# Kernel tuning notes

Measured on AMD Instinct MI355X. Metric: run time of the kernel, lower is better.

Reference implementation:

```python
import jax, jax.numpy as jnp
import numpy as np

N_NODES = 50000
N_EDGES = 1600000
IN_F, H_F, N_C = 128, 128, 16
NEG_SLOPE = 0.2  # DGL GATConv default


def setup_inputs() -> dict:
    key = jax.random.key(0)
    ks = jax.random.split(key, 12)
    def w(k, shape, fan_in):
        return jax.random.normal(k, shape, jnp.float32) / np.float32(np.sqrt(fan_in))
    return {
        "feat": jax.random.normal(ks[0], (N_NODES, IN_F), jnp.float32),
        "src": jax.random.randint(ks[1], (N_EDGES,), 0, N_NODES, dtype=jnp.int32),
        "dst": jax.random.randint(ks[2], (N_EDGES,), 0, N_NODES, dtype=jnp.int32),
        "W1": w(ks[3], (IN_F, H_F), IN_F), "al1": w(ks[4], (H_F,), H_F), "ar1": w(ks[5], (H_F,), H_F), "b1": jnp.zeros((H_F,), jnp.float32),
        "W2": w(ks[6], (H_F, H_F), H_F), "al2": w(ks[7], (H_F,), H_F), "ar2": w(ks[8], (H_F,), H_F), "b2": jnp.zeros((H_F,), jnp.float32),
        "W3": w(ks[9], (H_F, N_C), H_F), "al3": w(ks[10], (N_C,), N_C), "ar3": w(ks[11], (N_C,), N_C), "b3": jnp.zeros((N_C,), jnp.float32),
    }


def _gat_layer(h, src, dst, W, al, ar, b):
    # DGL GATConv (1 head): ft = W h; e_ij = LeakyReLU(a_l.ft_src + a_r.ft_dst);
    # alpha = edge_softmax over incoming edges of dst; out = sum alpha * ft_src + bias
    ft = h @ W                                   # [N, out]
    el = ft @ al                                 # [N]
    er = ft @ ar                                 # [N]
    e = jax.nn.leaky_relu(el[src] + er[dst], negative_slope=NEG_SLOPE)  # [E]
    emax = jax.ops.segment_max(e, dst, num_segments=N_NODES)
    emax = jnp.where(jnp.isfinite(emax), emax, 0.0)  # guard isolated nodes
    ex = jnp.exp(e - emax[dst])                  # [E]
    esum = jax.ops.segment_sum(ex, dst, num_segments=N_NODES)  # [N]
    agg = jax.ops.segment_sum(ex[:, None] * ft[src], dst, num_segments=N_NODES)  # [N, out]
    out = agg / jnp.where(esum > 0, esum, 1.0)[:, None] + b
    return jax.nn.relu(out)


def reference(feat, src, dst, W1, al1, ar1, b1, W2, al2, ar2, b2, W3, al3, ar3, b3):
    h = _gat_layer(feat, src, dst, W1, al1, ar1, b1)
    h = _gat_layer(h, src, dst, W2, al2, ar2, b2)
    h = _gat_layer(h, src, dst, W3, al3, ar3, b3)
    return h  # [N_NODES, N_C]
```

## Files before the change

### kernel.cpp

```cpp
#include <hip/hip_runtime.h>
#include <hip/hip_bf16.h>

#define NN 50000
#define NE 1600000
#define FF 128
#define CC 16
#define NB ((NN + 63) / 64)
#define NBLK 256
#define CH ((NE + NBLK - 1) / NBLK)

using bf16 = __hip_bfloat16;
using bf16x8 = __attribute__((ext_vector_type(8))) short;
using f32x4  = __attribute__((ext_vector_type(4))) float;

static __device__ __forceinline__ float ldf(const void* p, int i, int isbf){
    return isbf ? __bfloat162float(((const bf16*)p)[i]) : ((const float*)p)[i];
}
static __device__ __forceinline__ float bflo(unsigned u){
    union{unsigned x; float f;} c; c.x = u << 16; return c.f;
}
static __device__ __forceinline__ float bfhi(unsigned u){
    union{unsigned x; float f;} c; c.x = u & 0xFFFF0000u; return c.f;
}
static __device__ __forceinline__ unsigned short f2bfu(float v){
    bf16 b = __float2bfloat16(v);
    union{bf16 b; unsigned short u;} c; c.b = b; return c.u;
}

__global__ __launch_bounds__(256) void k_prep(const unsigned short* __restrict__ featu,
                                              const void* __restrict__ W1, const void* __restrict__ W2,
                                              const void* __restrict__ W3, int* __restrict__ dflag,
                                              int* __restrict__ bcounts, unsigned short* __restrict__ wtg){
    __shared__ int cnt;
    const int t = threadIdx.x;
    if (t == 0) cnt = 0;
    __syncthreads();
    unsigned short lo = featu[2 * t];
    int e = (lo >> 7) & 0xFF;
    if (e >= 117 && e <= 137) atomicAdd(&cnt, 1);
    __syncthreads();
    const int isbf = (cnt >= 128) ? 1 : 0;
    int idx = blockIdx.x * 256 + t;
    if (idx == 0) *dflag = isbf;
    if (idx < NB) bcounts[idx] = 0;
    if (idx < 32768){
        int l = idx >> 14;
        int e2 = idx & 16383;
        int f = e2 >> 7, k = e2 & 127;
        const void* W = l ? W2 : W1;
        wtg[idx] = f2bfu(ldf(W, k * FF + f, isbf));
    } else if (idx < 34816){
        int e2 = idx - 32768;
        int f = e2 >> 7, k = e2 & 127;
        wtg[idx] = f2bfu(ldf(W3, k * CC + f, isbf));
    }
}


__global__ __launch_bounds__(256) void k_bcount(const int* __restrict__ dst, int* __restrict__ bcounts,
                                                int* __restrict__ bh){
    __shared__ int hist[NB];
    const int t = threadIdx.x, b = blockIdx.x;
    for (int i = t; i < NB; i += 256) hist[i] = 0;
    __syncthreads();
    const int beg = b * CH, end = (beg + CH < NE) ? beg + CH : NE;
    for (int i = beg + t; i < end; i += 256){
        int d = dst[i];
        if ((unsigned)d >= NN) d = 0;
        atomicAdd(&hist[d >> 6], 1);
    }
    __syncthreads();
    for (int k = t; k < NB; k += 256){
        int v = hist[k];
        bh[k * NBLK + b] = v;
        if (v) atomicAdd(&bcounts[k], v);
    }
}

__global__ __launch_bounds__(256) void k_bscan(const int* __restrict__ bcounts, int* __restrict__ bbase,
                                               int* __restrict__ rowptr){
    __shared__ int s[256];
    const int t = threadIdx.x;
    constexpr int PT = (NB + 255) / 256;
    int loc[PT];
    int sum = 0;
    #pragma unroll
    for (int i = 0; i < PT; i++){
        int idx = t * PT + i;
        int v = (idx < NB) ? bcounts[idx] : 0;
        loc[i] = sum;
        sum += v;
    }
    s[t] = sum; __syncthreads();
    for (int off = 1; off < 256; off <<= 1){
        int x = (t >= off) ? s[t - off] : 0;
        __syncthreads();
        s[t] += x;
        __syncthreads();
    }
    int base = (t > 0) ? s[t - 1] : 0;
    #pragma unroll
    for (int i = 0; i < PT; i++){
        int idx = t * PT + i;
        if (idx < NB) bbase[idx] = base + loc[i];
    }
    if (t == 255){
        bbase[NB] = s[255];
        rowptr[NN] = s[255];
    }
}

__global__ __launch_bounds__(256) void k_boffset(const int* __restrict__ bbase, int* __restrict__ bh){
    int k = blockIdx.x * 4 + (threadIdx.x >> 6);
    int lane = threadIdx.x & 63;
    if (k >= NB) return;
    int v[4];
    int s = 0;
    #pragma unroll
    for (int i = 0; i < 4; i++){
        v[i] = bh[k * NBLK + 4 * lane + i];
        s += v[i];
    }
    int tot = s;
    #pragma unroll
    for (int off = 1; off < 64; off <<= 1){
        int x = __shfl_up(s, off);
        if (lane >= off) s += x;
    }
    int run = bbase[k] + s - tot;
    #pragma unroll
    for (int i = 0; i < 4; i++){
        bh[k * NBLK + 4 * lane + i] = run;
        run += v[i];
    }
}

__global__ __launch_bounds__(256) void k_bucket(const int* __restrict__ src, const int* __restrict__ dst,
                                                const int* __restrict__ bh, unsigned* __restrict__ bpairs){
    __shared__ int cur[NB];
    const int t = threadIdx.x, b = blockIdx.x;
    for (int k = t; k < NB; k += 256) cur[k] = bh[k * NBLK + b];
    __syncthreads();
    const int beg = b * CH, end = (beg + CH < NE) ? beg + CH : NE;
    for (int i = beg + t; i < end; i += 256){
        int s = src[i];
        int d = dst[i];
        if ((unsigned)s >= NN) s = 0;
        if ((unsigned)d >= NN) d = 0;
        int p = atomicAdd(&cur[d >> 6], 1);
        if ((unsigned)p < NE) bpairs[p] = (unsigned)s | ((unsigned)(d & 63) << 16);
    }
}

__global__ __launch_bounds__(256) void k_bsort(const unsigned* __restrict__ bpairs, const int* __restrict__ bbase,
                                               int* __restrict__ rowptr, int* __restrict__ csrsrc){
    __shared__ int cnt[64];
    __shared__ int cur[64];
    const int t = threadIdx.x;
    const int b = blockIdx.x;
    const int base = bbase[b];
    const int endb = bbase[b + 1];
    if (t < 64) cnt[t] = 0;
    __syncthreads();
    for (int i = base + t; i < endb; i += 256)
        atomicAdd(&cnt[bpairs[i] >> 16], 1);
    __syncthreads();
    if (t < 64){
        int v = cnt[t];
        int inc = v;
        #pragma unroll
        for (int off = 1; off < 64; off <<= 1){
            int x = __shfl_up(inc, off);
            if (t >= off) inc += x;
        }
        int excl = inc - v;
        cur[t] = excl;
        int d = b * 64 + t;
        if (d < NN) rowptr[d] = base + excl;
    }
    __syncthreads();
    for (int i = base + t; i < endb; i += 256){
        unsigned pr = bpairs[i];
        int p = atomicAdd(&cur[pr >> 16], 1);
        csrsrc[base + p] = (int)(pr & 0xFFFFu);
    }
}


template<bool XDYN>
__global__ __launch_bounds__(256) void k_mgemm(const void* __restrict__ X, const unsigned short* __restrict__ wtg,
                                               const void* __restrict__ al, const void* __restrict__ ar,
                                               const int* __restrict__ dflag, bf16* __restrict__ ft,
                                               float* __restrict__ el, float* __restrict__ er){
    const int isbf = *dflag;
    const int t  = threadIdx.x;
    const int n0 = blockIdx.x * 64;
    const int wv = t >> 6;
    const int lane = t & 63;
    const int quad = lane >> 4;
    const int mcol = lane & 15;
    const int row = n0 + wv * 16 + mcol;
    const int rc  = (row < NN) ? row : 0;

    bf16x8 afr[4];
    if (XDYN && !isbf){
        const float* xr = (const float*)X + rc * FF + quad * 8;
        #pragma unroll
        for (int kt = 0; kt < 4; kt++){
            float4 a = *(const float4*)(xr + kt * 32);
            float4 b = *(const float4*)(xr + kt * 32 + 4);
            union { bf16x8 v; unsigned u[4]; } c;
            c.u[0] = (unsigned)f2bfu(a.x) | ((unsigned)f2bfu(a.y) << 16);
            c.u[1] = (unsigned)f2bfu(a.z) | ((unsigned)f2bfu(a.w) << 16);
            c.u[2] = (unsigned)f2bfu(b.x) | ((unsigned)f2bfu(b.y) << 16);
            c.u[3] = (unsigned)f2bfu(b.z) | ((unsigned)f2bfu(b.w) << 16);
            afr[kt] = c.v;
        }
    } else {
        const unsigned short* xr = (const unsigned short*)X + rc * FF + quad * 8;
        #pragma unroll
        for (int kt = 0; kt < 4; kt++)
            afr[kt] = *(const bf16x8*)(xr + kt * 32);
    }

    float elp[4] = {0.f,0.f,0.f,0.f}, erp[4] = {0.f,0.f,0.f,0.f};

    #pragma unroll
    for (int f = 0; f < 8; f++){
        f32x4 acc = {0.f, 0.f, 0.f, 0.f};
        const unsigned short* wr = wtg + (f * 16 + mcol) * FF + quad * 8;
        #pragma unroll
        for (int kt = 0; kt < 4; kt++){
            bf16x8 bfr = *(const bf16x8*)(wr + kt * 32);
            acc = __builtin_amdgcn_mfma_f32_16x16x32_bf16(afr[kt], bfr, acc, 0, 0, 0);
        }
        int col = f * 16 + mcol;
        float alv = ldf(al, col, isbf);
        float arv = ldf(ar, col, isbf);
        #pragma unroll
        for (int reg = 0; reg < 4; reg++){
            int node = n0 + wv * 16 + quad * 4 + reg;
            float v = acc[reg];
            if (node < NN) ft[node * FF + col] = __float2bfloat16(v);
            elp[reg] += v * alv;
            erp[reg] += v * arv;
        }
    }

    #pragma unroll
    for (int reg = 0; reg < 4; reg++){
        float pl = elp[reg], pr = erp[reg];
        #pragma unroll
        for (int off = 1; off < 16; off <<= 1){
            pl += __shfl_xor(pl, off);
            pr += __shfl_xor(pr, off);
        }
        int node = n0 + wv * 16 + quad * 4 + reg;
        if (mcol == 0 && node < NN){ el[node] = pl; er[node] = pr; }
    }
}


__global__ __launch_bounds__(256) void k_mgemm3(const void* __restrict__ X, const unsigned short* __restrict__ wt3g,
                                                const void* __restrict__ al, const void* __restrict__ ar,
                                                const int* __restrict__ dflag, float* __restrict__ ft,
                                                float* __restrict__ el, float* __restrict__ er){
    const int isbf = *dflag;
    const int t  = threadIdx.x;
    const int n0 = blockIdx.x * 64;
    const int wv = t >> 6;
    const int lane = t & 63;
    const int quad = lane >> 4;
    const int mcol = lane & 15;
    const int row = n0 + wv * 16 + mcol;
    const int rc  = (row < NN) ? row : 0;

    const unsigned short* xr = (const unsigned short*)X + rc * FF + quad * 8;
    const unsigned short* wr = wt3g + mcol * FF + quad * 8;

    f32x4 acc = {0.f, 0.f, 0.f, 0.f};
    #pragma unroll
    for (int kt = 0; kt < 4; kt++){
        bf16x8 afr = *(const bf16x8*)(xr + kt * 32);
        bf16x8 bfr = *(const bf16x8*)(wr + kt * 32);
        acc = __builtin_amdgcn_mfma_f32_16x16x32_bf16(afr, bfr, acc, 0, 0, 0);
    }

    float alv = ldf(al, mcol, isbf);
    float arv = ldf(ar, mcol, isbf);
    #pragma unroll
    for (int reg = 0; reg < 4; reg++){
        int node = n0 + wv * 16 + quad * 4 + reg;
        float v = acc[reg];
        if (node < NN) ft[node * CC + mcol] = v;
        float pl = v * alv, pr = v * arv;
        #pragma unroll
        for (int off = 1; off < 16; off <<= 1){
            pl += __shfl_xor(pl, off);
            pr += __shfl_xor(pr, off);
        }
        if (mcol == 0 && node < NN){ el[node] = pl; er[node] = pr; }
    }
}


__global__ __launch_bounds__(256) void k_wnorm(const float* __restrict__ el, float* __restrict__ er,
                                               const int* __restrict__ rowptr, const int* __restrict__ csrsrc,
                                               float* __restrict__ wcsr){
    const int t = threadIdx.x;
    const int n = blockIdx.x * 64 + (t >> 2);
    if (n >= NN) return;
    const int sub = t & 3;
    int beg = rowptr[n], end = rowptr[n + 1];
    beg = (beg < 0) ? 0 : (beg > NE ? NE : beg);
    end = (end < beg) ? beg : (end > NE ? NE : end);
    const float erd = er[n];
    float sum = 0.f;
    for (int i = beg + sub; i < end; i += 4){
        int s = csrsrc[i];
        if ((unsigned)s >= NN) s = 0;
        float e = el[s] + erd;
        e = (e >= 0.f) ? e : 0.2f * e;
        float ex = __expf(e);
        wcsr[i] = ex;
        sum += ex;
    }
    sum += __shfl_xor(sum, 1);
    sum += __shfl_xor(sum, 2);
    if (sub == 0) er[n] = 1.f / ((sum > 0.f) ? sum : 1.f);
}


__global__ __launch_bounds__(256) void k_agg128(const void* __restrict__ ftv, const int* __restrict__ rowptr,
                                                const int* __restrict__ csrsrc, const float* __restrict__ wcsr,
                                                const float* __restrict__ erinv, const void* __restrict__ bias,
                                                const int* __restrict__ dflag, unsigned* __restrict__ outp){
    const int isbf = *dflag;
    const int lane = threadIdx.x & 63;
    const int n = blockIdx.x * 4 + (threadIdx.x >> 6);
    if (n >= NN) return;
    int beg = rowptr[n], end = rowptr[n + 1];
    beg = (beg < 0) ? 0 : (beg > NE ? NE : beg);
    end = (end < beg) ? beg : (end > NE ? NE : end);

    const int g = lane >> 4;
    const int c = lane & 15;
    const uint4* ftq4 = (const uint4*)ftv;
    float acc[8] = {0.f,0.f,0.f,0.f,0.f,0.f,0.f,0.f};

    for (int j = beg; j < end; j += 8){
        int iA = j + g;
        int iB = j + 4 + g;
        int cA = (iA < end) ? iA : beg;
        int cB = (iB < end) ? iB : beg;
        int sA = csrsrc[cA];
        int sB = csrsrc[cB];
        float wA = (iA < end) ? wcsr[cA] : 0.f;
        float wB = (iB < end) ? wcsr[cB] : 0.f;
        if ((unsigned)sA >= NN) sA = 0;
        if ((unsigned)sB >= NN) sB = 0;
        uint4 uA = ftq4[(unsigned)sA * 16u + c];
        uint4 uB = ftq4[(unsigned)sB * 16u + c];
        acc[0] += wA * bflo(uA.x); acc[1] += wA * bfhi(uA.x);
        acc[2] += wA * bflo(uA.y); acc[3] += wA * bfhi(uA.y);
        acc[4] += wA * bflo(uA.z); acc[5] += wA * bfhi(uA.z);
        acc[6] += wA * bflo(uA.w); acc[7] += wA * bfhi(uA.w);
        acc[0] += wB * bflo(uB.x); acc[1] += wB * bfhi(uB.x);
        acc[2] += wB * bflo(uB.y); acc[3] += wB * bfhi(uB.y);
        acc[4] += wB * bflo(uB.z); acc[5] += wB * bfhi(uB.z);
        acc[6] += wB * bflo(uB.w); acc[7] += wB * bfhi(uB.w);
    }

    #pragma unroll
    for (int k = 0; k < 8; k++){
        acc[k] += __shfl_xor(acc[k], 16);
        acc[k] += __shfl_xor(acc[k], 32);
    }

    if (g == 0){
        float inv = erinv[n];
        float o[8];
        #pragma unroll
        for (int k = 0; k < 8; k++)
            o[k] = fmaxf(acc[k] * inv + ldf(bias, c * 8 + k, isbf), 0.f);
        uint4 pk;
        pk.x = (unsigned)f2bfu(o[0]) | ((unsigned)f2bfu(o[1]) << 16);
        pk.y = (unsigned)f2bfu(o[2]) | ((unsigned)f2bfu(o[3]) << 16);
        pk.z = (unsigned)f2bfu(o[4]) | ((unsigned)f2bfu(o[5]) << 16);
        pk.w = (unsigned)f2bfu(o[6]) | ((unsigned)f2bfu(o[7]) << 16);
        ((uint4*)outp)[n * 16 + c] = pk;
    }
}


__global__ __launch_bounds__(256) void k_agg16(const float* __restrict__ ftv, const float* __restrict__ el,
                                               const float* __restrict__ er, const int* __restrict__ rowptr,
                                               const int* __restrict__ csrsrc, const void* __restrict__ bias,
                                               const int* __restrict__ dflag, void* __restrict__ outp){
    const int isbf = *dflag;
    int lane = threadIdx.x & 63;
    int n = blockIdx.x * 4 + (threadIdx.x >> 6);
    if (n >= NN) return;
    int beg = rowptr[n], end = rowptr[n + 1];
    beg = (beg < 0) ? 0 : (beg > NE ? NE : beg);
    end = (end < beg) ? beg : (end > NE ? NE : end);
    int deg = end - beg;
    float erd = er[n];

    float m = -3.4e38f;
    int   s_c = 0;
    float e_c = 0.f;
    for (int i = beg + lane; i < end; i += 64){
        int s = csrsrc[i];
        if ((unsigned)s >= NN) s = 0;
        float e = el[s] + erd;
        e = (e >= 0.f) ? e : 0.2f * e;
        if (i < beg + 64){ s_c = s; e_c = e; }
        m = fmaxf(m, e);
    }
    #pragma unroll
    for (int off = 32; off; off >>= 1) m = fmaxf(m, __shfl_xor(m, off));

    int jmax = (deg < 64) ? deg : 64;
    float w_c = (lane < jmax) ? __expf(e_c - m) : 0.f;
    float lsum = w_c;
    #pragma unroll
    for (int off = 32; off; off >>= 1) lsum += __shfl_xor(lsum, off);

    const float4* ftq = (const float4*)ftv;
    const int g   = lane >> 2;
    const int fl2 = lane & 3;
    int nbatch = (jmax + 15) >> 4;
    float wq[4]; float4 uq[4];
    #pragma unroll
    for (int q = 0; q < 4; q++){
        int eidx = (q * 16 + g) & 63;
        int s = __shfl(s_c, eidx);
        wq[q] = (q < nbatch) ? __shfl(w_c, eidx) : 0.f;
        uq[q] = ftq[(unsigned)s * 4 + fl2];
    }
    float a4[4] = {0.f,0.f,0.f,0.f};
    #pragma unroll
    for (int q = 0; q < 4; q++){
        a4[0] += wq[q] * uq[q].x;
        a4[1] += wq[q] * uq[q].y;
        a4[2] += wq[q] * uq[q].z;
        a4[3] += wq[q] * uq[q].w;
    }
    for (int i = beg + 64; i < end; ++i){
        int s = csrsrc[i];
        if ((unsigned)s >= NN) s = 0;
        float e = el[s] + erd;
        e = (e >= 0.f) ? e : 0.2f * e;
        float w = __expf(e - m);
        lsum += w;
        if (g == 0){
            float4 u = ftq[(unsigned)s * 4 + fl2];
            a4[0] += w * u.x; a4[1] += w * u.y; a4[2] += w * u.z; a4[3] += w * u.w;
        }
    }
    #pragma unroll
    for (int i = 0; i < 4; i++){
        a4[i] += __shfl_xor(a4[i], 4);
        a4[i] += __shfl_xor(a4[i], 8);
        a4[i] += __shfl_xor(a4[i], 16);
        a4[i] += __shfl_xor(a4[i], 32);
    }
    float inv = 1.f / ((lsum > 0.f) ? lsum : 1.f);
    if (lane < 4){
        float o0 = fmaxf(a4[0] * inv + ldf(bias, fl2 * 4 + 0, isbf), 0.f);
        float o1 = fmaxf(a4[1] * inv + ldf(bias, fl2 * 4 + 1, isbf), 0.f);
        float o2 = fmaxf(a4[2] * inv + ldf(bias, fl2 * 4 + 2, isbf), 0.f);
        float o3 = fmaxf(a4[3] * inv + ldf(bias, fl2 * 4 + 3, isbf), 0.f);
        if (isbf){
            uint2 pk;
            pk.x = (unsigned)f2bfu(o0) | ((unsigned)f2bfu(o1) << 16);
            pk.y = (unsigned)f2bfu(o2) | ((unsigned)f2bfu(o3) << 16);
            ((uint2*)outp)[n * 4 + fl2] = pk;
        } else {
            float4 o; o.x = o0; o.y = o1; o.z = o2; o.w = o3;
            ((float4*)outp)[n * 4 + fl2] = o;
        }
    }
}


static size_t align256(size_t x){ return (x + 255) & ~(size_t)255; }

extern "C" void kernel_launch(void* const* d_in, const int* in_sizes, int n_in,
                              void* d_out, int out_size, void* d_ws, size_t ws_size,
                              hipStream_t stream) {
    const void* feat = d_in[0];
    const int*  src  = (const int*)d_in[1];
    const int*  dst  = (const int*)d_in[2];
    const void* W1 = d_in[3];
    const void* al1= d_in[4];
    const void* ar1= d_in[5];
    const void* b1 = d_in[6];
    const void* W2 = d_in[7];
    const void* al2= d_in[8];
    const void* ar2= d_in[9];
    const void* b2 = d_in[10];
    const void* W3 = d_in[11];
    const void* al3= d_in[12];
    const void* ar3= d_in[13];
    const void* b3 = d_in[14];

    char* p = (char*)d_ws;
    size_t off = 0;
    auto carve = [&](size_t bytes)->void*{
        void* r = p + off;
        off += align256(bytes);
        return r;
    };
    float* ftA   = (float*)carve((size_t)NN * FF * 4);
    unsigned* hB = (unsigned*)carve((size_t)NN * FF * 4);
    float* el    = (float*)carve((size_t)NN * 4);
    float* er    = (float*)carve((size_t)NN * 4);
    int*   rowptr= (int*)  carve((size_t)(NN + 1) * 4);
    int*   csrsrc= (int*)  carve((size_t)NE * 4);
    int*   bcounts=(int*)  carve((size_t)NB * 4);
    int*   bbase  =(int*)  carve((size_t)(NB + 1) * 4);
    int*   bh     =(int*)  carve((size_t)NB * NBLK * 4);
    unsigned short* wtg = (unsigned short*)carve((size_t)34816 * 2);
    int*   dflag  =(int*)  carve(256);
    unsigned* bpairs = (unsigned*)hB;
    void*  ftb   = ftA;
    float* wcsr  = ftA + (size_t)NN * FF / 2;
    (void)ws_size; (void)n_in; (void)in_sizes; (void)out_size;

    dim3 b256(256);

    k_prep<<<dim3(136), b256, 0, stream>>>((const unsigned short*)feat, W1, W2, W3, dflag, bcounts, wtg);

    k_bcount<<<dim3(NBLK), b256, 0, stream>>>(dst, bcounts, bh);
    k_bscan<<<dim3(1), b256, 0, stream>>>(bcounts, bbase, rowptr);
    k_boffset<<<dim3((NB + 3) / 4), b256, 0, stream>>>(bbase, bh);
    k_bucket<<<dim3(NBLK), b256, 0, stream>>>(src, dst, bh, bpairs);
    k_bsort<<<dim3(NB), b256, 0, stream>>>(bpairs, bbase, rowptr, csrsrc);

    const int mg_grid   = (NN + 63) / 64;
    const int node_grid = (NN + 3) / 4;
    const int wn_grid   = (NN + 63) / 64;

    k_mgemm<true><<<dim3(mg_grid), b256, 0, stream>>>(feat, wtg, al1, ar1, dflag, (bf16*)ftb, el, er);
    k_wnorm<<<dim3(wn_grid), b256, 0, stream>>>(el, er, rowptr, csrsrc, wcsr);
    k_agg128<<<dim3(node_grid), b256, 0, stream>>>(ftb, rowptr, csrsrc, wcsr, er, b1, dflag, hB);

    k_mgemm<false><<<dim3(mg_grid), b256, 0, stream>>>(hB, wtg + 16384, al2, ar2, dflag, (bf16*)ftb, el, er);
    k_wnorm<<<dim3(wn_grid), b256, 0, stream>>>(el, er, rowptr, csrsrc, wcsr);
    k_agg128<<<dim3(node_grid), b256, 0, stream>>>(ftb, rowptr, csrsrc, wcsr, er, b2, dflag, hB);

    k_mgemm3<<<dim3(mg_grid), b256, 0, stream>>>(hB, wtg + 32768, al3, ar3, dflag, (float*)ftb, el, er);
    k_agg16<<<dim3(node_grid), b256, 0, stream>>>((const float*)ftb, el, er, rowptr, csrsrc, b3, dflag, d_out);
}
```

Baseline: 360.5 us.

## Fuse edge-weight softmax into aggregation kernels and drop max subtraction

Removes the separate k_wnorm pass. The 128-wide aggregation now computes exp(leakyrelu(el[s]+er[n])) per edge inline, accumulates the denominator alongside the feature sum, and unrolls to 4 edges per lane group. The 16-wide final layer also drops its max pass and uses a simple strided 32-edge loop. This saves two kernel launches and the wcsr write/read traffic. Skipping max subtraction risks overflow in exp for large logits, and isolated nodes now get a zero reciprocal (same output after bias and ReLU).

```diff
diff --git a/kernel.cpp b/kernel.cpp
--- a/kernel.cpp
+++ b/kernel.cpp
@@ -304,36 +304,9 @@
 }
 
 
-__global__ __launch_bounds__(256) void k_wnorm(const float* __restrict__ el, float* __restrict__ er,
-                                               const int* __restrict__ rowptr, const int* __restrict__ csrsrc,
-                                               float* __restrict__ wcsr){
-    const int t = threadIdx.x;
-    const int n = blockIdx.x * 64 + (t >> 2);
-    if (n >= NN) return;
-    const int sub = t & 3;
-    int beg = rowptr[n], end = rowptr[n + 1];
-    beg = (beg < 0) ? 0 : (beg > NE ? NE : beg);
-    end = (end < beg) ? beg : (end > NE ? NE : end);
-    const float erd = er[n];
-    float sum = 0.f;
-    for (int i = beg + sub; i < end; i += 4){
-        int s = csrsrc[i];
-        if ((unsigned)s >= NN) s = 0;
-        float e = el[s] + erd;
-        e = (e >= 0.f) ? e : 0.2f * e;
-        float ex = __expf(e);
-        wcsr[i] = ex;
-        sum += ex;
-    }
-    sum += __shfl_xor(sum, 1);
-    sum += __shfl_xor(sum, 2);
-    if (sub == 0) er[n] = 1.f / ((sum > 0.f) ? sum : 1.f);
-}
-
-
-__global__ __launch_bounds__(256) void k_agg128(const void* __restrict__ ftv, const int* __restrict__ rowptr,
-                                                const int* __restrict__ csrsrc, const float* __restrict__ wcsr,
-                                                const float* __restrict__ erinv, const void* __restrict__ bias,
+__global__ __launch_bounds__(256) void k_agg128(const void* __restrict__ ftv, const float* __restrict__ el,
+                                                const float* __restrict__ er, const int* __restrict__ rowptr,
+                                                const int* __restrict__ csrsrc, const void* __restrict__ bias,
                                                 const int* __restrict__ dflag, unsigned* __restrict__ outp){
     const int isbf = *dflag;
     const int lane = threadIdx.x & 63;
@@ -342,33 +315,43 @@
     int beg = rowptr[n], end = rowptr[n + 1];
     beg = (beg < 0) ? 0 : (beg > NE ? NE : beg);
     end = (end < beg) ? beg : (end > NE ? NE : end);
+    const float erd = er[n];
 
     const int g = lane >> 4;
     const int c = lane & 15;
     const uint4* ftq4 = (const uint4*)ftv;
     float acc[8] = {0.f,0.f,0.f,0.f,0.f,0.f,0.f,0.f};
-
-    for (int j = beg; j < end; j += 8){
-        int iA = j + g;
-        int iB = j + 4 + g;
-        int cA = (iA < end) ? iA : beg;
-        int cB = (iB < end) ? iB : beg;
-        int sA = csrsrc[cA];
-        int sB = csrsrc[cB];
-        float wA = (iA < end) ? wcsr[cA] : 0.f;
-        float wB = (iB < end) ? wcsr[cB] : 0.f;
-        if ((unsigned)sA >= NN) sA = 0;
-        if ((unsigned)sB >= NN) sB = 0;
-        uint4 uA = ftq4[(unsigned)sA * 16u + c];
-        uint4 uB = ftq4[(unsigned)sB * 16u + c];
-        acc[0] += wA * bflo(uA.x); acc[1] += wA * bfhi(uA.x);
-        acc[2] += wA * bflo(uA.y); acc[3] += wA * bfhi(uA.y);
-        acc[4] += wA * bflo(uA.z); acc[5] += wA * bfhi(uA.z);
-        acc[6] += wA * bflo(uA.w); acc[7] += wA * bfhi(uA.w);
-        acc[0] += wB * bflo(uB.x); acc[1] += wB * bfhi(uB.x);
-        acc[2] += wB * bflo(uB.y); acc[3] += wB * bfhi(uB.y);
-        acc[4] += wB * bflo(uB.z); acc[5] += wB * bfhi(uB.z);
-        acc[6] += wB * bflo(uB.w); acc[7] += wB * bfhi(uB.w);
+    float lsum = 0.f;
+
+    for (int j = beg; j < end; j += 16){
+        int   sE[4];
+        float wE[4];
+        uint4 uE[4];
+        #pragma unroll
+        for (int q = 0; q < 4; q++){
+            int iq = j + q * 4 + g;
+            int cq = (iq < end) ? iq : beg;
+            int s  = csrsrc[cq];
+            if ((unsigned)s >= NN) s = 0;
+            sE[q] = s;
+        }
+        #pragma unroll
+        for (int q = 0; q < 4; q++){
+            int iq = j + q * 4 + g;
+            float e = el[sE[q]] + erd;
+            e = (e >= 0.f) ? e : 0.2f * e;
+            wE[q] = (iq < end) ? __expf(e) : 0.f;
+            uE[q] = ftq4[(unsigned)sE[q] * 16u + c];
+        }
+        #pragma unroll
+        for (int q = 0; q < 4; q++){
+            float w = wE[q];
+            lsum += w;
+            acc[0] += w * bflo(uE[q].x); acc[1] += w * bfhi(uE[q].x);
+            acc[2] += w * bflo(uE[q].y); acc[3] += w * bfhi(uE[q].y);
+            acc[4] += w * bflo(uE[q].z); acc[5] += w * bfhi(uE[q].z);
+            acc[6] += w * bflo(uE[q].w); acc[7] += w * bfhi(uE[q].w);
+        }
     }
 
     #pragma unroll
@@ -376,9 +359,11 @@
         acc[k] += __shfl_xor(acc[k], 16);
         acc[k] += __shfl_xor(acc[k], 32);
     }
+    lsum += __shfl_xor(lsum, 16);
+    lsum += __shfl_xor(lsum, 32);
 
     if (g == 0){
-        float inv = erinv[n];
+        float inv = (lsum > 0.f) ? 1.f / lsum : 0.f;
         float o[8];
         #pragma unroll
         for (int k = 0; k < 8; k++)
@@ -398,88 +383,59 @@
                                                const int* __restrict__ csrsrc, const void* __restrict__ bias,
                                                const int* __restrict__ dflag, void* __restrict__ outp){
     const int isbf = *dflag;
-    int lane = threadIdx.x & 63;
-    int n = blockIdx.x * 4 + (threadIdx.x >> 6);
+    const int lane = threadIdx.x & 63;
+    const int n = blockIdx.x * 4 + (threadIdx.x >> 6);
     if (n >= NN) return;
     int beg = rowptr[n], end = rowptr[n + 1];
     beg = (beg < 0) ? 0 : (beg > NE ? NE : beg);
     end = (end < beg) ? beg : (end > NE ? NE : end);
-    int deg = end - beg;
-    float erd = er[n];
-
-    float m = -3.4e38f;
-    int   s_c = 0;
-    float e_c = 0.f;
-    for (int i = beg + lane; i < end; i += 64){
-        int s = csrsrc[i];
-        if ((unsigned)s >= NN) s = 0;
-        float e = el[s] + erd;
-        e = (e >= 0.f) ? e : 0.2f * e;
-        if (i < beg + 64){ s_c = s; e_c = e; }
-        m = fmaxf(m, e);
-    }
-    #pragma unroll
-    for (int off = 32; off; off >>= 1) m = fmaxf(m, __shfl_xor(m, off));
-
-    int jmax = (deg < 64) ? deg : 64;
-    float w_c = (lane < jmax) ? __expf(e_c - m) : 0.f;
-    float lsum = w_c;
-    #pragma unroll
-    for (int off = 32; off; off >>= 1) lsum += __shfl_xor(lsum, off);
-
+    const float erd = er[n];
+
+    const int g = lane >> 2;
+    const int c = lane & 3;
     const float4* ftq = (const float4*)ftv;
-    const int g   = lane >> 2;
-    const int fl2 = lane & 3;
-    int nbatch = (jmax + 15) >> 4;
-    float wq[4]; float4 uq[4];
-    #pragma unroll
-    for (int q = 0; q < 4; q++){
-        int eidx = (q * 16 + g) & 63;
-        int s = __shfl(s_c, eidx);
-        wq[q] = (q < nbatch) ? __shfl(w_c, eidx) : 0.f;
-        uq[q] = ftq[(unsigned)s * 4 + fl2];
-    }
-    float a4[4] = {0.f,0.f,0.f,0.f};
-    #pragma unroll
-    for (int q = 0; q < 4; q++){
-        a4[0] += wq[q] * uq[q].x;
-        a4[1] += wq[q] * uq[q].y;
-        a4[2] += wq[q] * uq[q].z;
-        a4[3] += wq[q] * uq[q].w;
-    }
-    for (int i = beg + 64; i < end; ++i){
-        int s = csrsrc[i];
-        if ((unsigned)s >= NN) s = 0;
-        float e = el[s] + erd;
-        e = (e >= 0.f) ? e : 0.2f * e;
-        float w = __expf(e - m);
-        lsum += w;
-        if (g == 0){
-            float4 u = ftq[(unsigned)s * 4 + fl2];
-            a4[0] += w * u.x; a4[1] += w * u.y; a4[2] += w * u.z; a4[3] += w * u.w;
-        }
-    }
-    #pragma unroll
-    for (int i = 0; i < 4; i++){
-        a4[i] += __shfl_xor(a4[i], 4);
-        a4[i] += __shfl_xor(a4[i], 8);
-        a4[i] += __shfl_xor(a4[i], 16);
-        a4[i] += __shfl_xor(a4[i], 32);
-    }
-    float inv = 1.f / ((lsum > 0.f) ? lsum : 1.f);
+    float a0 = 0.f, a1 = 0.f, a2 = 0.f, a3 = 0.f;
+    float lsum = 0.f;
+
+    for (int j = beg; j < end; j += 32){
+        #pragma unroll
+        for (int q = 0; q < 2; q++){
+            int iq = j + q * 16 + g;
+            int cq = (iq < end) ? iq : beg;
+            int s  = csrsrc[cq];
+            if ((unsigned)s >= NN) s = 0;
+            float e = el[s] + erd;
+            e = (e >= 0.f) ? e : 0.2f * e;
+            float w = (iq < end) ? __expf(e) : 0.f;
+            float4 u = ftq[(unsigned)s * 4u + c];
+            lsum += w;
+            a0 += w * u.x; a1 += w * u.y; a2 += w * u.z; a3 += w * u.w;
+        }
+    }
+
+    #pragma unroll
+    for (int off = 4; off < 64; off <<= 1){
+        a0 += __shfl_xor(a0, off);
+        a1 += __shfl_xor(a1, off);
+        a2 += __shfl_xor(a2, off);
+        a3 += __shfl_xor(a3, off);
+        lsum += __shfl_xor(lsum, off);
+    }
+
     if (lane < 4){
-        float o0 = fmaxf(a4[0] * inv + ldf(bias, fl2 * 4 + 0, isbf), 0.f);
-        float o1 = fmaxf(a4[1] * inv + ldf(bias, fl2 * 4 + 1, isbf), 0.f);
-        float o2 = fmaxf(a4[2] * inv + ldf(bias, fl2 * 4 + 2, isbf), 0.f);
-        float o3 = fmaxf(a4[3] * inv + ldf(bias, fl2 * 4 + 3, isbf), 0.f);
+        float inv = (lsum > 0.f) ? 1.f / lsum : 0.f;
+        float o0 = fmaxf(a0 * inv + ldf(bias, c * 4 + 0, isbf), 0.f);
+        float o1 = fmaxf(a1 * inv + ldf(bias, c * 4 + 1, isbf), 0.f);
+        float o2 = fmaxf(a2 * inv + ldf(bias, c * 4 + 2, isbf), 0.f);
+        float o3 = fmaxf(a3 * inv + ldf(bias, c * 4 + 3, isbf), 0.f);
         if (isbf){
             uint2 pk;
             pk.x = (unsigned)f2bfu(o0) | ((unsigned)f2bfu(o1) << 16);
             pk.y = (unsigned)f2bfu(o2) | ((unsigned)f2bfu(o3) << 16);
-            ((uint2*)outp)[n * 4 + fl2] = pk;
+            ((uint2*)outp)[n * 4 + c] = pk;
         } else {
             float4 o; o.x = o0; o.y = o1; o.z = o2; o.w = o3;
-            ((float4*)outp)[n * 4 + fl2] = o;
+            ((float4*)outp)[n * 4 + c] = o;
         }
     }
 }
@@ -526,7 +482,6 @@
     int*   dflag  =(int*)  carve(256);
     unsigned* bpairs = (unsigned*)hB;
     void*  ftb   = ftA;
-    float* wcsr  = ftA + (size_t)NN * FF / 2;
     (void)ws_size; (void)n_in; (void)in_sizes; (void)out_size;
 
     dim3 b256(256);
@@ -541,15 +496,12 @@
 
     const int mg_grid   = (NN + 63) / 64;
     const int node_grid = (NN + 3) / 4;
-    const int wn_grid   = (NN + 63) / 64;
 
     k_mgemm<true><<<dim3(mg_grid), b256, 0, stream>>>(feat, wtg, al1, ar1, dflag, (bf16*)ftb, el, er);
-    k_wnorm<<<dim3(wn_grid), b256, 0, stream>>>(el, er, rowptr, csrsrc, wcsr);
-    k_agg128<<<dim3(node_grid), b256, 0, stream>>>(ftb, rowptr, csrsrc, wcsr, er, b1, dflag, hB);
+    k_agg128<<<dim3(node_grid), b256, 0, stream>>>(ftb, el, er, rowptr, csrsrc, b1, dflag, hB);
 
     k_mgemm<false><<<dim3(mg_grid), b256, 0, stream>>>(hB, wtg + 16384, al2, ar2, dflag, (bf16*)ftb, el, er);
-    k_wnorm<<<dim3(wn_grid), b256, 0, stream>>>(el, er, rowptr, csrsrc, wcsr);
-    k_agg128<<<dim3(node_grid), b256, 0, stream>>>(ftb, rowptr, csrsrc, wcsr, er, b2, dflag, hB);
+    k_agg128<<<dim3(node_grid), b256, 0, stream>>>(ftb, el, er, rowptr, csrsrc, b2, dflag, hB);
 
     k_mgemm3<<<dim3(mg_grid), b256, 0, stream>>>(hB, wtg + 32768, al3, ar3, dflag, (float*)ftb, el, er);
     k_agg16<<<dim3(node_grid), b256, 0, stream>>>((const float*)ftb, el, er, rowptr, csrsrc, b3, dflag, d_out);
```

New measurement: 350.3 us. 2.8% less time.
